# Optimization experiments

Measured on AMD Instinct MI355X. Metric: run time of the kernel, lower is better.

Reference implementation:

```python
import jax, jax.numpy as jnp
import numpy as np

DIN = 256
T = 16                      # sample_duration
NSCALE, NRATIO = 6, 3
ANCHOR_NUM = 15             # placements of durations [16,12,8] in T=16: 1+5+9
NC_SCORE = NSCALE * NRATIO * ANCHOR_NUM * 2      # 540
NC_BBOX = NSCALE * NRATIO * ANCHOR_NUM * T * 4   # 17280
NC_SCORE16 = NSCALE * NRATIO * 2                 # 36
NC_BBOX16 = NSCALE * NRATIO * 4                  # 72
B, H, W = 4, 14, 14


def conv3d(x, w, b, padding):
    y = jax.lax.conv_general_dilated(
        x, w, window_strides=(1, 1, 1), padding=padding,
        dimension_numbers=('NCDHW', 'OIDHW', 'NCDHW'))
    return y + b[None, :, None, None, None]


def setup_inputs() -> dict:
    key = jax.random.key(0)
    ks = jax.random.split(key, 12)
    hid = DIN * 2
    s = 0.02
    return {
        'base_feat': jax.random.normal(ks[0], (B, DIN, T, H, W), jnp.float32),
        'im_info': jnp.ones((B, 3), jnp.float32) * 224.0,
        'gt_boxes': jax.random.uniform(ks[1], (B, 10, 7), jnp.float32),
        'gt_rois': jax.random.uniform(ks[2], (B, 10, 7), jnp.float32),
        'conv_w': jax.random.normal(ks[3], (hid, DIN, 3, 3, 3), jnp.float32) * s,
        'conv_b': jnp.zeros((hid,), jnp.float32),
        'cls_w': jax.random.normal(ks[4], (NC_SCORE, hid, T, 1, 1), jnp.float32) * s,
        'cls_b': jnp.zeros((NC_SCORE,), jnp.float32),
        'bbox_w': jax.random.normal(ks[5], (NC_BBOX, hid, T, 1, 1), jnp.float32) * s,
        'bbox_b': jnp.zeros((NC_BBOX,), jnp.float32),
        'cls16_w': jax.random.normal(ks[6], (NC_SCORE16, hid, T, 1, 1), jnp.float32) * s,
        'cls16_b': jnp.zeros((NC_SCORE16,), jnp.float32),
        'bbox16_w': jax.random.normal(ks[7], (NC_BBOX16, hid, T, 1, 1), jnp.float32) * s,
        'bbox16_b': jnp.zeros((NC_BBOX16,), jnp.float32),
    }


def _softmax_pairs(score, nc):
    # torch reshape2d(x,2) -> softmax(dim=1) -> reshape2d(x,nc)
    b, c, h, w = score.shape
    s = score.reshape(b, 2, (c * h) // 2, w)
    p = jax.nn.softmax(s, axis=1)
    return p.reshape(b, nc, h, w)


def reference(base_feat, im_info, gt_boxes, gt_rois,
              conv_w, conv_b, cls_w, cls_b, bbox_w, bbox_b,
              cls16_w, cls16_b, bbox16_w, bbox16_b):
    pad1 = [(1, 1), (1, 1), (1, 1)]
    rpn_conv1 = jax.nn.relu(conv3d(base_feat, conv_w, conv_b, pad1))
    # heads: kernel (T,1,1), VALID -> depth collapses to 1; squeeze(2)
    rpn_cls_score = conv3d(rpn_conv1, cls_w, cls_b, 'VALID').squeeze(2)      # [B,540,H,W]
    rpn_bbox_pred = conv3d(rpn_conv1, bbox_w, bbox_b, 'VALID').squeeze(2)    # [B,17280,H,W]
    rpn_cls_prob = _softmax_pairs(rpn_cls_score, NC_SCORE)
    rpn_cls_16 = conv3d(rpn_conv1, cls16_w, cls16_b, 'VALID').squeeze(2)     # [B,36,H,W]
    rpn_bbox_16 = conv3d(rpn_conv1, bbox16_w, bbox16_b, 'VALID').squeeze(2)  # [B,72,H,W]
    rpn_cls_prob_16 = _softmax_pairs(rpn_cls_16, NC_SCORE16)
    return (rpn_cls_prob, rpn_bbox_pred, rpn_cls_prob_16, rpn_bbox_16)
```

## Files before the change

### kernel.cpp

```cpp
#include <hip/hip_runtime.h>
#include <hip/hip_bf16.h>
#include <stdint.h>

typedef __attribute__((ext_vector_type(4))) float f32x4;
typedef __attribute__((ext_vector_type(4))) unsigned int u32x4;
typedef __bf16 v8bf __attribute__((ext_vector_type(8)));

#define GLL16(gp, lp) __builtin_amdgcn_global_load_lds( \
    (const __attribute__((address_space(1))) unsigned int*)(const void*)(gp), \
    (__attribute__((address_space(3))) unsigned int*)(void*)(lp), 16, 0, 0)

__device__ __forceinline__ unsigned pkbf(float a, float b) {
  return __builtin_amdgcn_perm(__float_as_uint(b), __float_as_uint(a), 0x07060302u);
}

#define OB1 423360
#define OB2 13970880
#define OB3 13999104

#define WS_XPAD   0
#define XPAD_GUARD_ELEMS 8192
#define WS_W1P    9519104
#define WS_X2T    16596992
#define WS_CLSS   31277056
#define WS_CLS16S 32970496
#define WS_BIAS2  33083392

__global__ void k_zero(u32x4* __restrict__ p) {
  p[blockIdx.x * 256 + threadIdx.x] = (u32x4){0u, 0u, 0u, 0u};
}

__global__ void k_fill_xpad(const float* __restrict__ bf, __hip_bfloat16* __restrict__ xp) {
  __shared__ float tile[64][65];
  int spb = blockIdx.x, cib = blockIdx.y, b = blockIdx.z;
  int t = threadIdx.x;
  int c0 = t >> 6;
  int sp_l = t & 63;
  const float* src = bf + (size_t)(b * 256 + cib * 64) * 3136 + spb * 64;
#pragma unroll
  for (int i = 0; i < 16; ++i) {
    int ci_l = i * 4 + c0;
    tile[ci_l][sp_l] = src[ci_l * 3136 + sp_l];
  }
  __syncthreads();
  int ci_l = t & 63;
#pragma unroll
  for (int i = 0; i < 16; ++i) {
    int spl = i * 4 + c0;
    int sp = spb * 64 + spl;
    int tt = sp / 196; int rr = sp - tt * 196;
    int y = rr / 14;   int x = rr - y * 14;
    int s = b * 4608 + (tt + 1) * 256 + (y + 1) * 16 + (x + 1);
    xp[(size_t)(32 + s) * 256 + cib * 64 + ci_l] = __float2bfloat16(tile[ci_l][spl]);
  }
}

__global__ void k_pack_w1(const float* __restrict__ cw, __hip_bfloat16* __restrict__ w1p) {
  int i = blockIdx.x * 256 + threadIdx.x;
  int co = i / 6912; int rem = i - co * 6912;
  int d = rem >> 8;  int ci = rem & 255;
  w1p[i] = __float2bfloat16(cw[co * 6912 + ci * 27 + d]);
}

__global__ void k_pack_bias2(const float* __restrict__ cb, const float* __restrict__ bb,
                             const float* __restrict__ c16, const float* __restrict__ b16,
                             float* __restrict__ bias2) {
  int i = blockIdx.x * 256 + threadIdx.x;
  if (i >= 18048) return;
  float v = 0.f;
  if (i < 540) v = cb[i];
  else if (i < 17820) v = bb[i - 540];
  else if (i < 17856) v = c16[i - 17820];
  else if (i < 17928) v = b16[i - 17856];
  bias2[i] = v;
}

__global__ __launch_bounds__(256, 2) void k_gemm1(
    const __hip_bfloat16* __restrict__ W1p,
    const __hip_bfloat16* __restrict__ Xp,
    const float* __restrict__ conv_b,
    __hip_bfloat16* __restrict__ X2T) {
  __shared__ short lA[128 * 64];
  __shared__ short lB[128 * 64];
  const int tid = threadIdx.x;
  const int ntile = blockIdx.x, mtile = blockIdx.y;
  const int lane = tid & 63, wave = tid >> 6;
  const int wm = wave & 1, wn = wave >> 1;

  long gA[4]; long gB[4];
#pragma unroll
  for (int i = 0; i < 4; ++i) {
    int c = i * 256 + tid;
    int row = c >> 3, pos = c & 7;
    int kc = pos ^ (row & 7);
    gA[i] = (long)(mtile * 128 + row) * 6912 + kc * 8;
    int col = ntile * 128 + row;
    int bi = col >> 12, rem = col & 4095;
    gB[i] = (long)(bi * 4608 + rem) * 256 + kc * 8;
  }
  f32x4 acc[4][4] = {};

  for (int d = 0; d < 27; ++d) {
    int dt = d / 9; int r9 = d - dt * 9; int dy = r9 / 3; int dx = r9 - dy * 3;
    long offd = (long)(dt * 256 + (dy - 1) * 16 + (dx - 1)) * 256;
    int kd = d * 256;
    for (int ci0 = 0; ci0 < 256; ci0 += 64) {
#pragma unroll
      for (int i = 0; i < 4; ++i) {
        GLL16(W1p + gA[i] + (kd + ci0), &lA[(i * 256 + tid) * 8]);
        GLL16(Xp + gB[i] + offd + ci0, &lB[(i * 256 + tid) * 8]);
      }
      __syncthreads();
#pragma unroll
      for (int ks = 0; ks < 2; ++ks) {
        v8bf af[4], bfr[4];
#pragma unroll
        for (int mi = 0; mi < 4; ++mi) {
          int row = wm * 64 + mi * 16 + (lane & 15);
          int ch = (ks * 4 + (lane >> 4)) ^ (row & 7);
          af[mi] = *(const v8bf*)&lA[row * 64 + ch * 8];
        }
#pragma unroll
        for (int ni = 0; ni < 4; ++ni) {
          int row = wn * 64 + ni * 16 + (lane & 15);
          int ch = (ks * 4 + (lane >> 4)) ^ (row & 7);
          bfr[ni] = *(const v8bf*)&lB[row * 64 + ch * 8];
        }
#pragma unroll
        for (int mi = 0; mi < 4; ++mi)
#pragma unroll
          for (int ni = 0; ni < 4; ++ni)
            acc[mi][ni] = __builtin_amdgcn_mfma_f32_16x16x32_bf16(af[mi], bfr[ni], acc[mi][ni], 0, 0, 0);
      }
      __syncthreads();
    }
  }
#pragma unroll
  for (int ni = 0; ni < 4; ++ni) {
    int col = ntile * 128 + wn * 64 + ni * 16 + (lane & 15);
    int bi = col >> 12, rem = col & 4095;
    int tt = rem >> 8, p2 = rem & 255;
    int yq = p2 >> 4, xq = p2 & 15;
    if (yq < 1 || yq > 14 || xq < 1 || xq > 14) continue;
    int n2 = bi * 196 + (yq - 1) * 14 + (xq - 1);
#pragma unroll
    for (int mi = 0; mi < 4; ++mi) {
#pragma unroll
      for (int rg = 0; rg < 4; ++rg) {
        int co = mtile * 128 + wm * 64 + mi * 16 + (lane >> 4) * 4 + rg;
        float v = acc[mi][ni][rg] + conv_b[co];
        v = fmaxf(v, 0.f);
        X2T[(size_t)n2 * 8192 + co * 16 + tt] = __float2bfloat16(v);
      }
    }
  }
}

__global__ __launch_bounds__(256, 2) void k_gemm2(
    const float* __restrict__ cls_w, const float* __restrict__ bbox_w,
    const float* __restrict__ cls16_w, const float* __restrict__ bbox16_w,
    const __hip_bfloat16* __restrict__ X2T, const float* __restrict__ bias2,
    float* __restrict__ out, float* __restrict__ cls_s, float* __restrict__ cls16_s) {
  __shared__ short lA[128 * 64];
  __shared__ short lB[128 * 64];
  const int tid = threadIdx.x;
  const int ntile = blockIdx.x, mtile = blockIdx.y;
  const int lane = tid & 63, wave = tid >> 6;
  const int wm = wave & 1, wn = wave >> 1;

  const int r = tid >> 1, h = tid & 1;
  const float* rowptr;
  {
    int o = mtile * 128 + r;
    if (o >= 17928) o = 0;
    if (o < 540) rowptr = cls_w + (size_t)o * 8192;
    else if (o < 17820) rowptr = bbox_w + (size_t)(o - 540) * 8192;
    else if (o < 17856) rowptr = cls16_w + (size_t)(o - 17820) * 8192;
    else rowptr = bbox16_w + (size_t)(o - 17856) * 8192;
    rowptr += h * 32;
  }
  long gB[4];
#pragma unroll
  for (int i = 0; i < 4; ++i) {
    int c = i * 256 + tid;
    int row = c >> 3, pos = c & 7;
    int kc = pos ^ (row & 7);
    gB[i] = (long)(ntile * 128 + row) * 8192 + kc * 8;
  }
  f32x4 acc[4][4] = {};

  for (int k0 = 0; k0 < 8192; k0 += 64) {
#pragma unroll
    for (int i = 0; i < 4; ++i)
      GLL16(X2T + gB[i] + k0, &lB[(i * 256 + tid) * 8]);
    const float4* p = (const float4*)(rowptr + k0);
    float4 v[8];
#pragma unroll
    for (int j = 0; j < 8; ++j) v[j] = p[j];
#pragma unroll
    for (int j = 0; j < 4; ++j) {
      u32x4 w;
      w.x = pkbf(v[2 * j].x, v[2 * j].y);
      w.y = pkbf(v[2 * j].z, v[2 * j].w);
      w.z = pkbf(v[2 * j + 1].x, v[2 * j + 1].y);
      w.w = pkbf(v[2 * j + 1].z, v[2 * j + 1].w);
      int pos = (h * 4 + j) ^ (r & 7);
      *(u32x4*)&lA[r * 64 + pos * 8] = w;
    }
    __syncthreads();
#pragma unroll
    for (int ks = 0; ks < 2; ++ks) {
      v8bf af[4], bfr[4];
#pragma unroll
      for (int mi = 0; mi < 4; ++mi) {
        int row = wm * 64 + mi * 16 + (lane & 15);
        int ch = (ks * 4 + (lane >> 4)) ^ (row & 7);
        af[mi] = *(const v8bf*)&lA[row * 64 + ch * 8];
      }
#pragma unroll
      for (int ni = 0; ni < 4; ++ni) {
        int row = wn * 64 + ni * 16 + (lane & 15);
        int ch = (ks * 4 + (lane >> 4)) ^ (row & 7);
        bfr[ni] = *(const v8bf*)&lB[row * 64 + ch * 8];
      }
#pragma unroll
      for (int mi = 0; mi < 4; ++mi)
#pragma unroll
        for (int ni = 0; ni < 4; ++ni)
          acc[mi][ni] = __builtin_amdgcn_mfma_f32_16x16x32_bf16(af[mi], bfr[ni], acc[mi][ni], 0, 0, 0);
    }
    __syncthreads();
  }
#pragma unroll
  for (int ni = 0; ni < 4; ++ni) {
    int col = ntile * 128 + wn * 64 + ni * 16 + (lane & 15);
    if (col >= 784) continue;
    int bi = col / 196, yx = col - bi * 196;
#pragma unroll
    for (int mi = 0; mi < 4; ++mi) {
#pragma unroll
      for (int rg = 0; rg < 4; ++rg) {
        int o = mtile * 128 + wm * 64 + mi * 16 + (lane >> 4) * 4 + rg;
        if (o >= 17928) continue;
        float val = acc[mi][ni][rg] + bias2[o];
        if (o < 540) cls_s[o * 784 + col] = val;
        else if (o < 17820) out[OB1 + ((size_t)bi * 17280 + (o - 540)) * 196 + yx] = val;
        else if (o < 17856) cls16_s[(o - 17820) * 784 + col] = val;
        else out[OB3 + ((size_t)bi * 72 + (o - 17856)) * 196 + yx] = val;
      }
    }
  }
}

__global__ void k_softmax_pairs(const float* __restrict__ s, float* __restrict__ out,
                                int half, int nc, long obase) {
  int idx = blockIdx.x * 256 + threadIdx.x;
  if (idx >= half * 784) return;
  int i = idx / 784, col = idx - i * 784;
  float s0 = s[i * 784 + col];
  float s1 = s[(i + half) * 784 + col];
  float m = fmaxf(s0, s1);
  float e0 = __expf(s0 - m), e1 = __expf(s1 - m);
  float inv = 1.0f / (e0 + e1);
  int bi = col / 196, yx = col - bi * 196;
  out[obase + ((size_t)bi * nc + i) * 196 + yx] = e0 * inv;
  out[obase + ((size_t)bi * nc + i + half) * 196 + yx] = e1 * inv;
}

extern "C" void kernel_launch(void* const* d_in, const int* in_sizes, int n_in,
                              void* d_out, int out_size, void* d_ws, size_t ws_size,
                              hipStream_t stream) {
  const float* base_feat = (const float*)d_in[0];
  const float* conv_w = (const float*)d_in[4];
  const float* conv_b = (const float*)d_in[5];
  const float* cls_w = (const float*)d_in[6];
  const float* cls_b = (const float*)d_in[7];
  const float* bbox_w = (const float*)d_in[8];
  const float* bbox_b = (const float*)d_in[9];
  const float* cls16_w = (const float*)d_in[10];
  const float* cls16_b = (const float*)d_in[11];
  const float* bbox16_w = (const float*)d_in[12];
  const float* bbox16_b = (const float*)d_in[13];
  float* out = (float*)d_out;
  char* ws = (char*)d_ws;

  __hip_bfloat16* xpad = (__hip_bfloat16*)(ws + WS_XPAD);
  __hip_bfloat16* w1p = (__hip_bfloat16*)(ws + WS_W1P);
  __hip_bfloat16* x2t = (__hip_bfloat16*)(ws + WS_X2T);
  float* cls_s = (float*)(ws + WS_CLSS);
  float* cls16_s = (float*)(ws + WS_CLS16S);
  float* bias2 = (float*)(ws + WS_BIAS2);

  dim3 blk(256);
  k_zero<<<dim3(2324), blk, 0, stream>>>((u32x4*)(ws + WS_XPAD));
  k_fill_xpad<<<dim3(49, 4, 4), blk, 0, stream>>>(base_feat, xpad);
  k_pack_w1<<<dim3(13824), blk, 0, stream>>>(conv_w, w1p);
  k_pack_bias2<<<dim3(71), blk, 0, stream>>>(cls_b, bbox_b, cls16_b, bbox16_b, bias2);
  k_gemm1<<<dim3(128, 4), blk, 0, stream>>>(w1p, xpad + XPAD_GUARD_ELEMS, conv_b, x2t);
  k_gemm2<<<dim3(7, 141), blk, 0, stream>>>(cls_w, bbox_w, cls16_w, bbox16_w, x2t, bias2,
                                            out, cls_s, cls16_s);
  k_softmax_pairs<<<dim3(827), blk, 0, stream>>>(cls_s, out, 270, 540, 0L);
  k_softmax_pairs<<<dim3(56), blk, 0, stream>>>(cls16_s, out, 18, 36, (long)OB2);
}
```

Before: 1.537 ms.

## Retile conv GEMM to 64 rows, widen head GEMM to per-batch 416-column tiles

```diff
diff --git a/kernel.cpp b/kernel.cpp
--- a/kernel.cpp
+++ b/kernel.cpp
@@ -75,30 +75,36 @@
   bias2[i] = v;
 }
 
-__global__ __launch_bounds__(256, 2) void k_gemm1(
+__global__ __launch_bounds__(256, 4) void k_gemm1(
     const __hip_bfloat16* __restrict__ W1p,
     const __hip_bfloat16* __restrict__ Xp,
     const float* __restrict__ conv_b,
     __hip_bfloat16* __restrict__ X2T) {
-  __shared__ short lA[128 * 64];
+  __shared__ short lA[64 * 64];
   __shared__ short lB[128 * 64];
   const int tid = threadIdx.x;
   const int ntile = blockIdx.x, mtile = blockIdx.y;
   const int lane = tid & 63, wave = tid >> 6;
   const int wm = wave & 1, wn = wave >> 1;
 
-  long gA[4]; long gB[4];
+  long gA[2]; long gB[4];
+#pragma unroll
+  for (int i = 0; i < 2; ++i) {
+    int c = i * 256 + tid;
+    int row = c >> 3, pos = c & 7;
+    int kc = pos ^ (row & 7);
+    gA[i] = (long)(mtile * 64 + row) * 6912 + kc * 8;
+  }
 #pragma unroll
   for (int i = 0; i < 4; ++i) {
     int c = i * 256 + tid;
     int row = c >> 3, pos = c & 7;
     int kc = pos ^ (row & 7);
-    gA[i] = (long)(mtile * 128 + row) * 6912 + kc * 8;
     int col = ntile * 128 + row;
     int bi = col >> 12, rem = col & 4095;
     gB[i] = (long)(bi * 4608 + rem) * 256 + kc * 8;
   }
-  f32x4 acc[4][4] = {};
+  f32x4 acc[2][4] = {};
 
   for (int d = 0; d < 27; ++d) {
     int dt = d / 9; int r9 = d - dt * 9; int dy = r9 / 3; int dx = r9 - dy * 3;
@@ -106,17 +112,18 @@
     int kd = d * 256;
     for (int ci0 = 0; ci0 < 256; ci0 += 64) {
 #pragma unroll
-      for (int i = 0; i < 4; ++i) {
+      for (int i = 0; i < 2; ++i)
         GLL16(W1p + gA[i] + (kd + ci0), &lA[(i * 256 + tid) * 8]);
+#pragma unroll
+      for (int i = 0; i < 4; ++i)
         GLL16(Xp + gB[i] + offd + ci0, &lB[(i * 256 + tid) * 8]);
-      }
       __syncthreads();
 #pragma unroll
       for (int ks = 0; ks < 2; ++ks) {
-        v8bf af[4], bfr[4];
-#pragma unroll
-        for (int mi = 0; mi < 4; ++mi) {
-          int row = wm * 64 + mi * 16 + (lane & 15);
+        v8bf af[2], bfr[4];
+#pragma unroll
+        for (int mi = 0; mi < 2; ++mi) {
+          int row = wm * 32 + mi * 16 + (lane & 15);
           int ch = (ks * 4 + (lane >> 4)) ^ (row & 7);
           af[mi] = *(const v8bf*)&lA[row * 64 + ch * 8];
         }
@@ -127,7 +134,7 @@
           bfr[ni] = *(const v8bf*)&lB[row * 64 + ch * 8];
         }
 #pragma unroll
-        for (int mi = 0; mi < 4; ++mi)
+        for (int mi = 0; mi < 2; ++mi)
 #pragma unroll
           for (int ni = 0; ni < 4; ++ni)
             acc[mi][ni] = __builtin_amdgcn_mfma_f32_16x16x32_bf16(af[mi], bfr[ni], acc[mi][ni], 0, 0, 0);
@@ -142,15 +149,15 @@
     int tt = rem >> 8, p2 = rem & 255;
     int yq = p2 >> 4, xq = p2 & 15;
     if (yq < 1 || yq > 14 || xq < 1 || xq > 14) continue;
-    int n2 = bi * 196 + (yq - 1) * 14 + (xq - 1);
-#pragma unroll
-    for (int mi = 0; mi < 4; ++mi) {
+    int n2p = bi * 208 + (yq - 1) * 14 + (xq - 1);
+#pragma unroll
+    for (int mi = 0; mi < 2; ++mi) {
 #pragma unroll
       for (int rg = 0; rg < 4; ++rg) {
-        int co = mtile * 128 + wm * 64 + mi * 16 + (lane >> 4) * 4 + rg;
+        int co = mtile * 64 + wm * 32 + mi * 16 + (lane >> 4) * 4 + rg;
         float v = acc[mi][ni][rg] + conv_b[co];
         v = fmaxf(v, 0.f);
-        X2T[(size_t)n2 * 8192 + co * 16 + tt] = __float2bfloat16(v);
+        X2T[(size_t)n2p * 8192 + co * 16 + tt] = __float2bfloat16(v);
       }
     }
   }
@@ -161,92 +168,97 @@
     const float* __restrict__ cls16_w, const float* __restrict__ bbox16_w,
     const __hip_bfloat16* __restrict__ X2T, const float* __restrict__ bias2,
     float* __restrict__ out, float* __restrict__ cls_s, float* __restrict__ cls16_s) {
-  __shared__ short lA[128 * 64];
-  __shared__ short lB[128 * 64];
+  __shared__ short lA[64 * 64];
+  __shared__ short lB[416 * 64];
   const int tid = threadIdx.x;
   const int ntile = blockIdx.x, mtile = blockIdx.y;
   const int lane = tid & 63, wave = tid >> 6;
   const int wm = wave & 1, wn = wave >> 1;
 
-  const int r = tid >> 1, h = tid & 1;
+  const int r = tid >> 2, q = tid & 3;
   const float* rowptr;
   {
-    int o = mtile * 128 + r;
+    int o = mtile * 64 + r;
     if (o >= 17928) o = 0;
     if (o < 540) rowptr = cls_w + (size_t)o * 8192;
     else if (o < 17820) rowptr = bbox_w + (size_t)(o - 540) * 8192;
     else if (o < 17856) rowptr = cls16_w + (size_t)(o - 17820) * 8192;
     else rowptr = bbox16_w + (size_t)(o - 17856) * 8192;
-    rowptr += h * 32;
-  }
-  long gB[4];
-#pragma unroll
-  for (int i = 0; i < 4; ++i) {
+    rowptr += q * 16;
+  }
+  const int pos0 = (q * 2) ^ (r & 7), pos1 = (q * 2 + 1) ^ (r & 7);
+
+  long gB[13];
+#pragma unroll
+  for (int i = 0; i < 13; ++i) {
     int c = i * 256 + tid;
     int row = c >> 3, pos = c & 7;
     int kc = pos ^ (row & 7);
-    gB[i] = (long)(ntile * 128 + row) * 8192 + kc * 8;
-  }
-  f32x4 acc[4][4] = {};
+    gB[i] = (long)(ntile * 416 + row) * 8192 + kc * 8;
+  }
+  f32x4 acc[2][13] = {};
+
+  float4 v0, v1, v2, v3;
+  {
+    const float4* p = (const float4*)rowptr;
+    v0 = p[0]; v1 = p[1]; v2 = p[2]; v3 = p[3];
+  }
 
   for (int k0 = 0; k0 < 8192; k0 += 64) {
 #pragma unroll
-    for (int i = 0; i < 4; ++i)
+    for (int i = 0; i < 13; ++i)
       GLL16(X2T + gB[i] + k0, &lB[(i * 256 + tid) * 8]);
-    const float4* p = (const float4*)(rowptr + k0);
-    float4 v[8];
-#pragma unroll
-    for (int j = 0; j < 8; ++j) v[j] = p[j];
-#pragma unroll
-    for (int j = 0; j < 4; ++j) {
-      u32x4 w;
-      w.x = pkbf(v[2 * j].x, v[2 * j].y);
-      w.y = pkbf(v[2 * j].z, v[2 * j].w);
-      w.z = pkbf(v[2 * j + 1].x, v[2 * j + 1].y);
-      w.w = pkbf(v[2 * j + 1].z, v[2 * j + 1].w);
-      int pos = (h * 4 + j) ^ (r & 7);
-      *(u32x4*)&lA[r * 64 + pos * 8] = w;
+    {
+      u32x4 w0, w1;
+      w0.x = pkbf(v0.x, v0.y); w0.y = pkbf(v0.z, v0.w);
+      w0.z = pkbf(v1.x, v1.y); w0.w = pkbf(v1.z, v1.w);
+      w1.x = pkbf(v2.x, v2.y); w1.y = pkbf(v2.z, v2.w);
+      w1.z = pkbf(v3.x, v3.y); w1.w = pkbf(v3.z, v3.w);
+      *(u32x4*)&lA[r * 64 + pos0 * 8] = w0;
+      *(u32x4*)&lA[r * 64 + pos1 * 8] = w1;
+    }
+    if (k0 + 64 < 8192) {
+      const float4* p = (const float4*)(rowptr + k0 + 64);
+      v0 = p[0]; v1 = p[1]; v2 = p[2]; v3 = p[3];
     }
     __syncthreads();
 #pragma unroll
     for (int ks = 0; ks < 2; ++ks) {
-      v8bf af[4], bfr[4];
-#pragma unroll
-      for (int mi = 0; mi < 4; ++mi) {
-        int row = wm * 64 + mi * 16 + (lane & 15);
+      v8bf af[2];
+#pragma unroll
+      for (int mi = 0; mi < 2; ++mi) {
+        int row = wm * 32 + mi * 16 + (lane & 15);
         int ch = (ks * 4 + (lane >> 4)) ^ (row & 7);
         af[mi] = *(const v8bf*)&lA[row * 64 + ch * 8];
       }
 #pragma unroll
-      for (int ni = 0; ni < 4; ++ni) {
-        int row = wn * 64 + ni * 16 + (lane & 15);
+      for (int ni = 0; ni < 13; ++ni) {
+        int row = wn * 208 + ni * 16 + (lane & 15);
         int ch = (ks * 4 + (lane >> 4)) ^ (row & 7);
-        bfr[ni] = *(const v8bf*)&lB[row * 64 + ch * 8];
-      }
-#pragma unroll
-      for (int mi = 0; mi < 4; ++mi)
-#pragma unroll
-        for (int ni = 0; ni < 4; ++ni)
-          acc[mi][ni] = __builtin_amdgcn_mfma_f32_16x16x32_bf16(af[mi], bfr[ni], acc[mi][ni], 0, 0, 0);
+        v8bf bfr = *(const v8bf*)&lB[row * 64 + ch * 8];
+        acc[0][ni] = __builtin_amdgcn_mfma_f32_16x16x32_bf16(af[0], bfr, acc[0][ni], 0, 0, 0);
+        acc[1][ni] = __builtin_amdgcn_mfma_f32_16x16x32_bf16(af[1], bfr, acc[1][ni], 0, 0, 0);
+      }
     }
     __syncthreads();
   }
-#pragma unroll
-  for (int ni = 0; ni < 4; ++ni) {
-    int col = ntile * 128 + wn * 64 + ni * 16 + (lane & 15);
-    if (col >= 784) continue;
-    int bi = col / 196, yx = col - bi * 196;
-#pragma unroll
-    for (int mi = 0; mi < 4; ++mi) {
+  const int batch = ntile * 2 + wn;
+#pragma unroll
+  for (int ni = 0; ni < 13; ++ni) {
+    int cib = ni * 16 + (lane & 15);
+    if (cib >= 196) continue;
+    int col = batch * 196 + cib;
+#pragma unroll
+    for (int mi = 0; mi < 2; ++mi) {
 #pragma unroll
       for (int rg = 0; rg < 4; ++rg) {
-        int o = mtile * 128 + wm * 64 + mi * 16 + (lane >> 4) * 4 + rg;
+        int o = mtile * 64 + wm * 32 + mi * 16 + (lane >> 4) * 4 + rg;
         if (o >= 17928) continue;
         float val = acc[mi][ni][rg] + bias2[o];
         if (o < 540) cls_s[o * 784 + col] = val;
-        else if (o < 17820) out[OB1 + ((size_t)bi * 17280 + (o - 540)) * 196 + yx] = val;
+        else if (o < 17820) out[OB1 + ((size_t)batch * 17280 + (o - 540)) * 196 + cib] = val;
         else if (o < 17856) cls16_s[(o - 17820) * 784 + col] = val;
-        else out[OB3 + ((size_t)bi * 72 + (o - 17856)) * 196 + yx] = val;
+        else out[OB3 + ((size_t)batch * 72 + (o - 17856)) * 196 + cib] = val;
       }
     }
   }
@@ -296,8 +308,8 @@
   k_fill_xpad<<<dim3(49, 4, 4), blk, 0, stream>>>(base_feat, xpad);
   k_pack_w1<<<dim3(13824), blk, 0, stream>>>(conv_w, w1p);
   k_pack_bias2<<<dim3(71), blk, 0, stream>>>(cls_b, bbox_b, cls16_b, bbox16_b, bias2);
-  k_gemm1<<<dim3(128, 4), blk, 0, stream>>>(w1p, xpad + XPAD_GUARD_ELEMS, conv_b, x2t);
-  k_gemm2<<<dim3(7, 141), blk, 0, stream>>>(cls_w, bbox_w, cls16_w, bbox16_w, x2t, bias2,
+  k_gemm1<<<dim3(128, 8), blk, 0, stream>>>(w1p, xpad + XPAD_GUARD_ELEMS, conv_b, x2t);
+  k_gemm2<<<dim3(2, 281), blk, 0, stream>>>(cls_w, bbox_w, cls16_w, bbox16_w, x2t, bias2,
                                             out, cls_s, cls16_s);
   k_softmax_pairs<<<dim3(827), blk, 0, stream>>>(cls_s, out, 270, 540, 0L);
   k_softmax_pairs<<<dim3(56), blk, 0, stream>>>(cls16_s, out, 18, 36, (long)OB2);
```

Result: faster. 1.496 ms (-2.7%).
